# Kernel tuning notes

Measured on AMD Instinct MI355X. Metric: run time of the kernel, lower is better.

Reference implementation:

```python
import jax, jax.numpy as jnp
import numpy as np

TAU = 2.0      # LIF time constant
EPS = 1e-5     # BatchNorm eps
ALPHA = 4.0    # sigmoid surrogate-gradient sharpness (spikingjelly default)

@jax.custom_vjp
def _spike(x):
    return (x >= 0.0).astype(x.dtype)

def _spike_fwd(x):
    return _spike(x), x

def _spike_bwd(x, g):
    s = jax.nn.sigmoid(ALPHA * x)
    return (g * ALPHA * s * (1.0 - s),)

_spike.defvjp(_spike_fwd, _spike_bwd)

def lif(x_seq, v_th=1.0):
    # Multi-step LIF with hard reset to 0, detach_reset=True, v[0]=0.
    # x_seq: (T, ...) ; scan over T.
    def step(v, x):
        v = v + (x - v) / TAU
        s = _spike(v - v_th)
        v = v * (1.0 - jax.lax.stop_gradient(s))  # detach_reset
        return v, s
    _, s_seq = jax.lax.scan(step, jnp.zeros_like(x_seq[0]), x_seq)
    return s_seq

def bn(x, gamma, beta, mean, var):
    # inference-mode BatchNorm2d on (T,B,C,H,W), params (C,)
    sh = (1, 1, -1, 1, 1)
    scale = gamma.reshape(sh) * jax.lax.rsqrt(var.reshape(sh) + EPS)
    return (x - mean.reshape(sh)) * scale + beta.reshape(sh)

def conv1x1(x, w):
    # 1x1 conv == channel matmul; x: (T,B,C,H,W), w: (Cout,Cin)
    return jnp.einsum('tbchw,dc->tbdhw', x, w)

def setup_inputs() -> dict:
    key = jax.random.key(0)
    ks = jax.random.split(key, 24)
    T, B, C, H, W = 4, 32, 384, 16, 16
    d = {}
    d['x'] = jax.random.normal(ks[0], (T, B, C, H, W), jnp.float32)
    for i, p in enumerate(['q', 'k', 'v']):
        base = 1 + 5 * i
        d[p + '_w'] = jax.random.normal(ks[base], (C, C), jnp.float32) * 0.05
        d[p + '_gamma'] = jax.random.uniform(ks[base + 1], (C,), jnp.float32) + 0.5
        d[p + '_beta'] = jax.random.normal(ks[base + 2], (C,), jnp.float32) * 0.1
        d[p + '_mean'] = jax.random.normal(ks[base + 3], (C,), jnp.float32) * 0.1
        d[p + '_var'] = jax.random.uniform(ks[base + 4], (C,), jnp.float32) + 0.5
    d['proj_w'] = jax.random.normal(ks[16], (C, C), jnp.float32) * 0.05
    d['proj_b'] = jax.random.normal(ks[17], (C,), jnp.float32) * 0.1
    d['proj_gamma'] = jax.random.uniform(ks[18], (C,), jnp.float32) + 0.5
    d['proj_beta'] = jax.random.normal(ks[19], (C,), jnp.float32) * 0.1
    d['proj_mean'] = jax.random.normal(ks[20], (C,), jnp.float32) * 0.1
    d['proj_var'] = jax.random.uniform(ks[21], (C,), jnp.float32) + 0.5
    d['num_heads'] = 8
    return d

def reference(x, q_w, q_gamma, q_beta, q_mean, q_var,
              k_w, k_gamma, k_beta, k_mean, k_var,
              v_w, v_gamma, v_beta, v_mean, v_var,
              proj_w, proj_b, proj_gamma, proj_beta, proj_mean, proj_var,
              num_heads):
    T, B, C, H, W = x.shape
    N = H * W
    Ch = C // num_heads
    identity = x
    xs = lif(x)  # shortcut_lif

    def branch(w, g, b, m, var_):
        o = lif(bn(conv1x1(xs, w), g, b, m, var_))  # (T,B,C,H,W), binary spikes
        # flatten(3).transpose(-1,-2).reshape(T,B,N,h,Ch).permute -> (T,B,h,N,Ch)
        return o.reshape(T, B, num_heads, Ch, N).transpose(0, 1, 2, 4, 3)

    q = branch(q_w, q_gamma, q_beta, q_mean, q_var)
    k = branch(k_w, k_gamma, k_beta, k_mean, k_var)
    v = branch(v_w, v_gamma, v_beta, v_mean, v_var)

    kv = (k * v).sum(axis=3, keepdims=True)      # (T,B,h,1,Ch) linear-attn reduce over N
    kv = lif(kv, v_th=0.5)                       # talking_heads_lif
    y = q * kv                                   # (T,B,h,N,Ch)
    y = y.transpose(0, 1, 2, 4, 3).reshape(T, B, C, H, W)
    y = conv1x1(y, proj_w) + proj_b.reshape(1, 1, -1, 1, 1)
    y = bn(y, proj_gamma, proj_beta, proj_mean, proj_var)
    return (y + identity, v)
```

## Files before the change

### kernel.cpp

```cpp
#include <hip/hip_runtime.h>

typedef unsigned short u16;
typedef unsigned char u8;
typedef signed char i8;
typedef int i32x4 __attribute__((ext_vector_type(4)));
typedef int i32x16 __attribute__((ext_vector_type(16)));
typedef float f32x4 __attribute__((ext_vector_type(4)));
typedef unsigned u32x4 __attribute__((ext_vector_type(4)));
typedef u8 u8x16 __attribute__((ext_vector_type(16)));

#define CHS 2097152L

__device__ __forceinline__ void gload16(const void* g, void* l) {
    __builtin_amdgcn_global_load_lds(
        (const __attribute__((address_space(1))) void*)g,
        (__attribute__((address_space(3))) void*)l, 16, 0, 0);
}

__global__ __launch_bounds__(256) void prep(const float* __restrict__ X, u8* __restrict__ Xt,
    const float* __restrict__ qw, const float* __restrict__ kw,
    const float* __restrict__ vw, const float* __restrict__ pw,
    i8* __restrict__ Wq, float* __restrict__ Sc, float* __restrict__ KVraw) {
    const int bid = blockIdx.x;
    if (bid < 768) {
        __shared__ __attribute__((aligned(16))) u8 s2[4][32][136];
        const int c0 = (bid % 3) * 128;
        const int n0 = ((bid / 3) & 7) * 32;
        const int b = bid / 24;
        const int n4 = (threadIdx.x & 7) << 2;
        const int cl0 = threadIdx.x >> 3;
        #pragma unroll
        for (int pass = 0; pass < 4; pass++) {
            const int c_l = cl0 + (pass << 5);
            f32x4 vm = {0.f, 0.f, 0.f, 0.f};
            #pragma unroll
            for (int t = 0; t < 4; t++) {
                f32x4 xv = __builtin_nontemporal_load(
                    (const f32x4*)&X[(((long)t * 32 + b) * 384 + c0 + c_l) * 256 + n0 + n4]);
                #pragma unroll
                for (int e = 0; e < 4; e++) {
                    vm[e] += (xv[e] - vm[e]) * 0.5f;
                    u8 sp = 0;
                    if (vm[e] >= 1.0f) { sp = 1; vm[e] = 0.f; }
                    s2[t][n4 + e][c_l] = sp;
                }
            }
        }
        __syncthreads();
        const int c16 = (threadIdx.x & 7) << 4;
        const int n = (threadIdx.x >> 3) & 31;
        const int cglob = c0 + c16;
        const int ch = cglob >> 6, off = cglob & 63;
        #pragma unroll
        for (int t = 0; t < 4; t++) {
            u8x16 v = *(const u8x16*)&s2[t][n][c16];
            *(u8x16*)&Xt[(long)ch * CHS + ((long)(b * 256 + n0 + n) * 4 + t) * 64 + off] = v;
        }
    } else {
        const int wv = bid - 768;
        const int w = threadIdx.x >> 6, lane = threadIdx.x & 63;
        const int r = wv * 4 + w;
        const int m = r / 384, d = r - m * 384;
        const float* srcs[4] = {qw, kw, vw, pw};
        const float* row = srcs[m] + (long)d * 384;
        float a[6]; float mx = 0.f;
        #pragma unroll
        for (int jj = 0; jj < 6; jj++) { a[jj] = row[lane + (jj << 6)]; mx = fmaxf(mx, fabsf(a[jj])); }
        #pragma unroll
        for (int off = 1; off < 64; off <<= 1) mx = fmaxf(mx, __shfl_xor(mx, off));
        float scale = mx * (1.f / 127.f);
        float sinv = mx > 0.f ? 127.f / mx : 0.f;
        if (lane == 0) Sc[r] = scale;
        i8* dstb = Wq + (long)(m == 3 ? 9 : m * 3) * 147456 + (long)d * 64;
        #pragma unroll
        for (int jj = 0; jj < 6; jj++) {
            float x = a[jj] * sinv;
            float q1 = rintf(x);         float r1 = x - q1;
            float q2 = rintf(r1 * 128.f); float r2 = r1 * 128.f - q2;
            float q3 = rintf(r2 * 128.f);
            int co = jj * 24576 + lane;
            dstb[co] = (i8)(int)q1;
            dstb[147456 + co] = (i8)(int)q2;
            if (m != 3) dstb[2 * 147456 + co] = (i8)(int)q3;
        }
        const int idx = wv * 256 + threadIdx.x;
        if (idx < 49152) KVraw[idx] = 0.f;
    }
}

template<int NL>
__device__ __forceinline__ void gemm_i8(const u8* __restrict__ A, const i8* __restrict__ B,
                                        char* lds8, int m0, int n0, i32x16 (&acc)[NL][2]) {
    const int tid = threadIdx.x, l = tid & 63, w = tid >> 6;
    const int wm = (w & 1) << 6, wn = (w >> 1) << 5;
    const int col = l & 31, kg = l >> 5;
    const int rA = tid >> 2, sl = tid & 3;
    const int cs = (sl ^ ((rA >> 1) & 3)) << 4;
    const u8* Ap = A + (long)(m0 + rA) * 64 + cs;
    const i8* Bp = B + (long)(n0 + rA) * 64 + cs;
    const int BUFSZ = (2 + NL) * 4096;
    char* dst = lds8 + tid * 16;

    gload16(Ap, dst);
    gload16(Ap + 4096, dst + 4096);
    #pragma unroll
    for (int p = 0; p < NL; p++)
        gload16(Bp + p * 147456, dst + 8192 + p * 4096);

    for (int ck = 0; ck < 6; ck++) {
        const int cur = ck & 1;
        if (ck < 5) {
            char* d = dst + (cur ^ 1) * BUFSZ;
            gload16(Ap + (ck + 1) * CHS, d);
            gload16(Ap + (ck + 1) * CHS + 4096, d + 4096);
            #pragma unroll
            for (int p = 0; p < NL; p++)
                gload16(Bp + p * 147456 + (ck + 1) * 24576, d + 8192 + p * 4096);
            if (NL == 3) asm volatile("s_waitcnt vmcnt(5)" ::: "memory");
            else         asm volatile("s_waitcnt vmcnt(4)" ::: "memory");
        } else {
            asm volatile("s_waitcnt vmcnt(0)" ::: "memory");
        }
        __builtin_amdgcn_s_barrier();
        __builtin_amdgcn_sched_barrier(0);
        char* base = lds8 + cur * BUFSZ;
        #pragma unroll
        for (int c = 0; c < 2; c++) {
            i32x4 af[2];
            #pragma unroll
            for (int i = 0; i < 2; i++) {
                int ra = wm + (i << 5) + col;
                int sa = ((2 * c + kg) ^ ((ra >> 1) & 3)) << 4;
                af[i] = *(const i32x4*)(base + ra * 64 + sa);
            }
            int rb = wn + col;
            int sb = ((2 * c + kg) ^ ((rb >> 1) & 3)) << 4;
            #pragma unroll
            for (int p = 0; p < NL; p++) {
                i32x4 bf = *(const i32x4*)(base + 8192 + p * 4096 + rb * 64 + sb);
                #pragma unroll
                for (int i = 0; i < 2; i++)
                    acc[p][i] = __builtin_amdgcn_mfma_i32_32x32x32_i8(af[i], bf, acc[p][i], 0, 0, 0);
            }
        }
        __builtin_amdgcn_sched_barrier(0);
        __builtin_amdgcn_s_barrier();
    }
}

__global__ __launch_bounds__(256, 4) void k2(
    const u8* __restrict__ Xt, const i8* __restrict__ Wq, const float* __restrict__ Sc,
    const float* __restrict__ g0, const float* __restrict__ b0, const float* __restrict__ m0_, const float* __restrict__ v0_,
    const float* __restrict__ g1, const float* __restrict__ b1, const float* __restrict__ m1_, const float* __restrict__ v1_,
    const float* __restrict__ g2, const float* __restrict__ b2, const float* __restrict__ m2_, const float* __restrict__ v2_,
    u8* __restrict__ oq, u8* __restrict__ ok, u8* __restrict__ ov, float* __restrict__ out1)
{
    __shared__ __attribute__((aligned(16))) char lds8[40960];
    const int bid = blockIdx.x;
    const int xcd = bid & 7, bi = bid >> 3;
    const int mt = (bi / 18) * 8 + xcd;
    const int sub = bi % 18;
    const int m0 = mt * 128, d0 = (sub % 6) * 64, br = sub / 6;
    const float* G  = br == 0 ? g0  : (br == 1 ? g1  : g2);
    const float* Be = br == 0 ? b0  : (br == 1 ? b1  : b2);
    const float* Mu = br == 0 ? m0_ : (br == 1 ? m1_ : m2_);
    const float* Va = br == 0 ? v0_ : (br == 1 ? v1_ : v2_);

    i32x16 acc[3][2];
    #pragma unroll
    for (int p = 0; p < 3; p++)
        #pragma unroll
        for (int i = 0; i < 2; i++)
            #pragma unroll
            for (int r = 0; r < 16; r++) acc[p][i][r] = 0;
    gemm_i8<3>(Xt, Wq + (long)br * 3 * 147456, lds8, m0, d0, acc);

    const int tid = threadIdx.x, l = tid & 63, w = tid >> 6;
    const int wm = (w & 1) << 6, wn = (w >> 1) << 5;
    const int col = l & 31;
    const int d = d0 + wn + col;
    const float scb = G[d] / sqrtf(Va[d] + 1e-5f);
    const float mu = Mu[d], be = Be[d];
    const float wsc = Sc[br * 384 + d];
    u8* tile8 = (u8*)lds8;
    const float c1 = 0.0078125f, c2 = 6.103515625e-05f;
    #pragma unroll
    for (int i = 0; i < 2; i++)
        #pragma unroll
        for (int q = 0; q < 4; q++) {
            float vm = 0.f;
            int mb = wm + (i << 5) + (q << 3) + ((l >> 5) << 2);
            #pragma unroll
            for (int t = 0; t < 4; t++) {
                int reg = q * 4 + t;
                float f = (float)acc[0][i][reg] + (float)acc[1][i][reg] * c1
                        + (float)acc[2][i][reg] * c2;
                float bn = (f * wsc - mu) * scb + be;
                vm += (bn - vm) * 0.5f;
                u8 s = 0;
                if (vm >= 1.0f) { s = 1; vm = 0.f; }
                tile8[(mb + t) * 80 + wn + col] = s;
            }
        }
    __syncthreads();
    u8* Out8 = br == 0 ? oq : (br == 1 ? ok : ov);
    const long rbase = (long)(d0 >> 6) * CHS + (long)m0 * 64;
    u32x4 w0 = *(const u32x4*)&tile8[(tid >> 2) * 80 + ((tid & 3) << 4)];
    u32x4 w1 = *(const u32x4*)&tile8[(64 + (tid >> 2)) * 80 + ((tid & 3) << 4)];
    *(u32x4*)(Out8 + rbase + tid * 16) = w0;
    *(u32x4*)(Out8 + rbase + 4096 + tid * 16) = w1;
    if (br == 2) {
        const int b = m0 >> 10, n_base = (m0 >> 2) & 255;
        const int dl4 = (tid & 15) << 2;
        const int d2 = d0 + dl4;
        const int h = d2 / 48, chn = d2 - h * 48;
        #pragma unroll
        for (int q = 0; q < 8; q++) {
            int mlq = (tid >> 4) + (q << 4);
            int t = mlq & 3, n = n_base + (mlq >> 2);
            f32x4 v;
            #pragma unroll
            for (int r = 0; r < 4; r++) v[r] = tile8[mlq * 80 + dl4 + r] ? 1.0f : 0.f;
            long gi = ((((long)t * 32 + b) * 8 + h) * 256 + n) * 48 + chn;
            __builtin_nontemporal_store(v, (f32x4*)&out1[gi]);
        }
    }
}

__global__ __launch_bounds__(384) void k3a(const u8* __restrict__ Ks, const u8* __restrict__ Vs,
                                           float* __restrict__ kv_raw) {
    const int b = blockIdx.y, nc = blockIdx.x;
    const int d4 = threadIdx.x * 4, t = threadIdx.y;
    const long cbase = (long)(d4 >> 6) * CHS + (d4 & 63);
    int cnt0 = 0, cnt1 = 0, cnt2 = 0, cnt3 = 0;
    for (int nl = 0; nl < 32; nl++) {
        const long row = ((long)b * 256 + nc * 32 + nl) * 4 + t;
        uchar4 kk = *(const uchar4*)&Ks[cbase + row * 64];
        uchar4 vv = *(const uchar4*)&Vs[cbase + row * 64];
        cnt0 += (kk.x & vv.x); cnt1 += (kk.y & vv.y);
        cnt2 += (kk.z & vv.z); cnt3 += (kk.w & vv.w);
    }
    float* dst = &kv_raw[((long)t * 32 + b) * 384 + d4];
    atomicAdd(dst + 0, (float)cnt0);
    atomicAdd(dst + 1, (float)cnt1);
    atomicAdd(dst + 2, (float)cnt2);
    atomicAdd(dst + 3, (float)cnt3);
}

__global__ __launch_bounds__(256, 4) void k4(
    const u8* __restrict__ Qs, const float* __restrict__ kv_raw,
    const i8* __restrict__ Pq, const float* __restrict__ Scp,
    const float* __restrict__ PB, const float* __restrict__ PG, const float* __restrict__ PBe,
    const float* __restrict__ PM, const float* __restrict__ PV,
    const float* __restrict__ X, float* __restrict__ O)
{
    __shared__ __attribute__((aligned(16))) char lds8[35328];
    u8* kvs_s = (u8*)(lds8 + 33792);
    const int bid = blockIdx.x;
    const int xcd = bid & 7, bi = bid >> 3;
    const int mt = (bi / 6) * 8 + xcd;
    const int m0 = mt * 128, e0 = (bi % 6) * 64;
    const int tid = threadIdx.x;
    const int b = m0 >> 10;

    for (int dd = tid; dd < 384; dd += 256) {
        float vm = 0.f;
        #pragma unroll
        for (int t = 0; t < 4; t++) {
            vm += (kv_raw[((long)t * 32 + b) * 384 + dd] - vm) * 0.5f;
            u8 sp = 0;
            if (vm >= 0.5f) { sp = 1; vm = 0.f; }
            kvs_s[t * 384 + dd] = sp;
        }
    }
    __syncthreads();

    i32x16 acc[2][2];
    #pragma unroll
    for (int p = 0; p < 2; p++)
        #pragma unroll
        for (int i = 0; i < 2; i++)
            #pragma unroll
            for (int r = 0; r < 16; r++) acc[p][i][r] = 0;
    const int l = tid & 63, w = tid >> 6;
    const int wm = (w & 1) << 6, wn = (w >> 1) << 5;
    const int col = l & 31, kg = l >> 5;
    const int rA = tid >> 2, sl = tid & 3;
    const int cs = (sl ^ ((rA >> 1) & 3)) << 4;
    const int tA = rA & 3;
    const u8* Ap = Qs + (long)(m0 + rA) * 64 + cs;
    const i8* Bp = Pq + (long)(e0 + rA) * 64 + cs;
    const int BUFSZ = 16384;
    char* dst = lds8 + tid * 16;
    {
        u32x4 mk = *(const u32x4*)&kvs_s[tA * 384 + cs];
        u32x4 q0 = *(const u32x4*)(Ap);
        u32x4 q1 = *(const u32x4*)(Ap + 4096);
        gload16(Bp, dst + 8192);
        gload16(Bp + 147456, dst + 12288);
        *(u32x4*)dst = q0 & mk;
        *(u32x4*)(dst + 4096) = q1 & mk;
    }
    __syncthreads();
    for (int ck = 0; ck < 6; ck++) {
        const int cur = ck & 1;
        u32x4 qn0, qn1, mk;
        char* dn = dst + (cur ^ 1) * BUFSZ;
        if (ck < 5) {
            mk = *(const u32x4*)&kvs_s[tA * 384 + (ck + 1) * 64 + cs];
            qn0 = *(const u32x4*)(Ap + (ck + 1) * CHS);
            qn1 = *(const u32x4*)(Ap + (ck + 1) * CHS + 4096);
            gload16(Bp + (ck + 1) * 24576, dn + 8192);
            gload16(Bp + 147456 + (ck + 1) * 24576, dn + 12288);
        }
        char* base = lds8 + cur * BUFSZ;
        #pragma unroll
        for (int c = 0; c < 2; c++) {
            i32x4 af[2];
            #pragma unroll
            for (int i = 0; i < 2; i++) {
                int ra = wm + (i << 5) + col;
                int sa = ((2 * c + kg) ^ ((ra >> 1) & 3)) << 4;
                af[i] = *(const i32x4*)(base + ra * 64 + sa);
            }
            int rb = wn + col;
            int sb = ((2 * c + kg) ^ ((rb >> 1) & 3)) << 4;
            #pragma unroll
            for (int p = 0; p < 2; p++) {
                i32x4 bf = *(const i32x4*)(base + 8192 + p * 4096 + rb * 64 + sb);
                #pragma unroll
                for (int i = 0; i < 2; i++)
                    acc[p][i] = __builtin_amdgcn_mfma_i32_32x32x32_i8(af[i], bf, acc[p][i], 0, 0, 0);
            }
        }
        if (ck < 5) {
            *(u32x4*)dn = qn0 & mk;
            *(u32x4*)(dn + 4096) = qn1 & mk;
        }
        __syncthreads();
    }

    const int e = e0 + wn + col;
    const float scb = PG[e] / sqrtf(PV[e] + 1e-5f);
    const float mu = PM[e], be = PBe[e], pbb = PB[e];
    const float wsc = Scp[e];
    float* smemf = (float*)lds8;
    const float c1 = 0.0078125f;
    #pragma unroll
    for (int i = 0; i < 2; i++)
        #pragma unroll
        for (int q = 0; q < 4; q++)
            #pragma unroll
            for (int t = 0; t < 4; t++) {
                int reg = q * 4 + t;
                float f = (float)acc[0][i][reg] + (float)acc[1][i][reg] * c1;
                float z = (f * wsc + pbb - mu) * scb + be;
                int m = wm + (i << 5) + (q << 3) + ((l >> 5) << 2) + t;
                smemf[(wn + col) * 132 + m] = z;
            }
    __syncthreads();
    const int n_base = (m0 >> 2) & 255;
    const int n_l = tid & 31;
    #pragma unroll
    for (int ei = 0; ei < 8; ei++) {
        int e_l = (tid >> 5) + (ei << 3);
        f32x4 v = *(const f32x4*)&smemf[e_l * 132 + (n_l << 2)];
        #pragma unroll
        for (int t = 0; t < 4; t++) {
            long gi = (((long)t * 32 + b) * 384 + e0 + e_l) * 256 + n_base + n_l;
            float xv = __builtin_nontemporal_load(&X[gi]);
            __builtin_nontemporal_store(v[t] + xv, &O[gi]);
        }
    }
}

extern "C" void kernel_launch(void* const* d_in, const int* in_sizes, int n_in,
                              void* d_out, int out_size, void* d_ws, size_t ws_size,
                              hipStream_t stream) {
    (void)in_sizes; (void)n_in; (void)out_size; (void)ws_size;
    const float* x   = (const float*)d_in[0];
    const float* qw  = (const float*)d_in[1];
    const float* qg  = (const float*)d_in[2];
    const float* qb  = (const float*)d_in[3];
    const float* qm  = (const float*)d_in[4];
    const float* qv  = (const float*)d_in[5];
    const float* kw  = (const float*)d_in[6];
    const float* kg  = (const float*)d_in[7];
    const float* kb  = (const float*)d_in[8];
    const float* km  = (const float*)d_in[9];
    const float* kv  = (const float*)d_in[10];
    const float* vw  = (const float*)d_in[11];
    const float* vg  = (const float*)d_in[12];
    const float* vb  = (const float*)d_in[13];
    const float* vm  = (const float*)d_in[14];
    const float* vv  = (const float*)d_in[15];
    const float* pw  = (const float*)d_in[16];
    const float* pb  = (const float*)d_in[17];
    const float* pg  = (const float*)d_in[18];
    const float* pbe = (const float*)d_in[19];
    const float* pm  = (const float*)d_in[20];
    const float* pv  = (const float*)d_in[21];

    float* out0 = (float*)d_out;
    float* out1 = out0 + 12582912;
    char*  ob   = (char*)d_out;
    u8*    Qs8  = (u8*)ob;
    u8*    Xt8  = (u8*)(ob + 12582912);
    char*  ws   = (char*)d_ws;
    u8*    Ks8  = (u8*)ws;
    u8*    Vs8  = (u8*)ws + 12582912;
    float* KVraw = (float*)(ws + 25165824);
    i8*    Wq    = (i8*)(ws + 25411584);
    float* Sc    = (float*)(ws + 27033600);

    hipLaunchKernelGGL(prep, dim3(1152), dim3(256), 0, stream, x, Xt8, qw, kw, vw, pw, Wq, Sc, KVraw);
    hipLaunchKernelGGL(k2, dim3(4608), dim3(256), 0, stream,
                       Xt8, Wq, Sc,
                       qg, qb, qm, qv,
                       kg, kb, km, kv,
                       vg, vb, vm, vv,
                       Qs8, Ks8, Vs8, out1);
    hipLaunchKernelGGL(k3a, dim3(8, 32), dim3(96, 4), 0, stream, Ks8, Vs8, KVraw);
    hipLaunchKernelGGL(k4, dim3(1536), dim3(256), 0, stream,
                       Qs8, KVraw, Wq + 9 * 147456L, Sc + 3 * 384, pb, pg, pbe, pm, pv, x, out0);
}
```

Baseline: 262.0 us.

## Fuse K·V spike-count reduction into the K/V GEMM blocks and drop k3a

The k2 kernel now uses 3072 blocks. Q blocks run the Q GEMM alone, and combined blocks run the K GEMM then the V GEMM back to back. The K and V spikes are kept in per-lane bitmasks, ANDed, popcounted per timestep into shared counters, and atomically added to kv_raw. This removes the K/V spike write-back to workspace and the separate k3a reduction launch. The cost is that K/V blocks now do two GEMMs serially, which makes the load uneven between Q and K/V blocks.

```diff
diff --git a/kernel.cpp b/kernel.cpp
--- a/kernel.cpp
+++ b/kernel.cpp
@@ -3,6 +3,7 @@
 typedef unsigned short u16;
 typedef unsigned char u8;
 typedef signed char i8;
+typedef unsigned u32;
 typedef int i32x4 __attribute__((ext_vector_type(4)));
 typedef int i32x16 __attribute__((ext_vector_type(16)));
 typedef float f32x4 __attribute__((ext_vector_type(4)));
@@ -153,98 +154,146 @@
     const float* __restrict__ g0, const float* __restrict__ b0, const float* __restrict__ m0_, const float* __restrict__ v0_,
     const float* __restrict__ g1, const float* __restrict__ b1, const float* __restrict__ m1_, const float* __restrict__ v1_,
     const float* __restrict__ g2, const float* __restrict__ b2, const float* __restrict__ m2_, const float* __restrict__ v2_,
-    u8* __restrict__ oq, u8* __restrict__ ok, u8* __restrict__ ov, float* __restrict__ out1)
+    u8* __restrict__ oq, float* __restrict__ kv_raw, float* __restrict__ out1)
 {
     __shared__ __attribute__((aligned(16))) char lds8[40960];
+    __shared__ int cnt_s[4][64];
     const int bid = blockIdx.x;
     const int xcd = bid & 7, bi = bid >> 3;
-    const int mt = (bi / 18) * 8 + xcd;
-    const int sub = bi % 18;
-    const int m0 = mt * 128, d0 = (sub % 6) * 64, br = sub / 6;
-    const float* G  = br == 0 ? g0  : (br == 1 ? g1  : g2);
-    const float* Be = br == 0 ? b0  : (br == 1 ? b1  : b2);
-    const float* Mu = br == 0 ? m0_ : (br == 1 ? m1_ : m2_);
-    const float* Va = br == 0 ? v0_ : (br == 1 ? v1_ : v2_);
-
-    i32x16 acc[3][2];
-    #pragma unroll
-    for (int p = 0; p < 3; p++)
-        #pragma unroll
-        for (int i = 0; i < 2; i++)
-            #pragma unroll
-            for (int r = 0; r < 16; r++) acc[p][i][r] = 0;
-    gemm_i8<3>(Xt, Wq + (long)br * 3 * 147456, lds8, m0, d0, acc);
-
+    const int mt = (bi / 12) * 8 + xcd;
+    const int sub = bi % 12;
+    const int m0 = mt * 128, d0 = (sub % 6) * 64;
+    const int role = sub / 6;
     const int tid = threadIdx.x, l = tid & 63, w = tid >> 6;
     const int wm = (w & 1) << 6, wn = (w >> 1) << 5;
     const int col = l & 31;
     const int d = d0 + wn + col;
-    const float scb = G[d] / sqrtf(Va[d] + 1e-5f);
-    const float mu = Mu[d], be = Be[d];
-    const float wsc = Sc[br * 384 + d];
+    const int b = m0 >> 10;
     u8* tile8 = (u8*)lds8;
     const float c1 = 0.0078125f, c2 = 6.103515625e-05f;
-    #pragma unroll
-    for (int i = 0; i < 2; i++)
-        #pragma unroll
-        for (int q = 0; q < 4; q++) {
-            float vm = 0.f;
-            int mb = wm + (i << 5) + (q << 3) + ((l >> 5) << 2);
-            #pragma unroll
-            for (int t = 0; t < 4; t++) {
-                int reg = q * 4 + t;
-                float f = (float)acc[0][i][reg] + (float)acc[1][i][reg] * c1
-                        + (float)acc[2][i][reg] * c2;
-                float bn = (f * wsc - mu) * scb + be;
-                vm += (bn - vm) * 0.5f;
-                u8 s = 0;
-                if (vm >= 1.0f) { s = 1; vm = 0.f; }
-                tile8[(mb + t) * 80 + wn + col] = s;
-            }
-        }
-    __syncthreads();
-    u8* Out8 = br == 0 ? oq : (br == 1 ? ok : ov);
-    const long rbase = (long)(d0 >> 6) * CHS + (long)m0 * 64;
-    u32x4 w0 = *(const u32x4*)&tile8[(tid >> 2) * 80 + ((tid & 3) << 4)];
-    u32x4 w1 = *(const u32x4*)&tile8[(64 + (tid >> 2)) * 80 + ((tid & 3) << 4)];
-    *(u32x4*)(Out8 + rbase + tid * 16) = w0;
-    *(u32x4*)(Out8 + rbase + 4096 + tid * 16) = w1;
-    if (br == 2) {
-        const int b = m0 >> 10, n_base = (m0 >> 2) & 255;
-        const int dl4 = (tid & 15) << 2;
-        const int d2 = d0 + dl4;
-        const int h = d2 / 48, chn = d2 - h * 48;
-        #pragma unroll
-        for (int q = 0; q < 8; q++) {
-            int mlq = (tid >> 4) + (q << 4);
-            int t = mlq & 3, n = n_base + (mlq >> 2);
-            f32x4 v;
-            #pragma unroll
-            for (int r = 0; r < 4; r++) v[r] = tile8[mlq * 80 + dl4 + r] ? 1.0f : 0.f;
-            long gi = ((((long)t * 32 + b) * 8 + h) * 256 + n) * 48 + chn;
-            __builtin_nontemporal_store(v, (f32x4*)&out1[gi]);
-        }
-    }
-}
-
-__global__ __launch_bounds__(384) void k3a(const u8* __restrict__ Ks, const u8* __restrict__ Vs,
-                                           float* __restrict__ kv_raw) {
-    const int b = blockIdx.y, nc = blockIdx.x;
-    const int d4 = threadIdx.x * 4, t = threadIdx.y;
-    const long cbase = (long)(d4 >> 6) * CHS + (d4 & 63);
-    int cnt0 = 0, cnt1 = 0, cnt2 = 0, cnt3 = 0;
-    for (int nl = 0; nl < 32; nl++) {
-        const long row = ((long)b * 256 + nc * 32 + nl) * 4 + t;
-        uchar4 kk = *(const uchar4*)&Ks[cbase + row * 64];
-        uchar4 vv = *(const uchar4*)&Vs[cbase + row * 64];
-        cnt0 += (kk.x & vv.x); cnt1 += (kk.y & vv.y);
-        cnt2 += (kk.z & vv.z); cnt3 += (kk.w & vv.w);
-    }
-    float* dst = &kv_raw[((long)t * 32 + b) * 384 + d4];
-    atomicAdd(dst + 0, (float)cnt0);
-    atomicAdd(dst + 1, (float)cnt1);
-    atomicAdd(dst + 2, (float)cnt2);
-    atomicAdd(dst + 3, (float)cnt3);
+
+    i32x16 acc[3][2];
+    if (role == 0) {
+        #pragma unroll
+        for (int p = 0; p < 3; p++)
+            #pragma unroll
+            for (int i = 0; i < 2; i++)
+                #pragma unroll
+                for (int r = 0; r < 16; r++) acc[p][i][r] = 0;
+        gemm_i8<3>(Xt, Wq, lds8, m0, d0, acc);
+        const float scb = g0[d] / sqrtf(v0_[d] + 1e-5f);
+        const float mu = m0_[d], be = b0[d];
+        const float wsc = Sc[d];
+        #pragma unroll
+        for (int i = 0; i < 2; i++)
+            #pragma unroll
+            for (int q = 0; q < 4; q++) {
+                float vm = 0.f;
+                int mb = wm + (i << 5) + (q << 3) + ((l >> 5) << 2);
+                #pragma unroll
+                for (int t = 0; t < 4; t++) {
+                    int reg = q * 4 + t;
+                    float f = (float)acc[0][i][reg] + (float)acc[1][i][reg] * c1
+                            + (float)acc[2][i][reg] * c2;
+                    float bn = (f * wsc - mu) * scb + be;
+                    vm += (bn - vm) * 0.5f;
+                    u8 s = 0;
+                    if (vm >= 1.0f) { s = 1; vm = 0.f; }
+                    tile8[(mb + t) * 80 + wn + col] = s;
+                }
+            }
+        __syncthreads();
+        const long rbase = (long)(d0 >> 6) * CHS + (long)m0 * 64;
+        u32x4 w0 = *(const u32x4*)&tile8[(tid >> 2) * 80 + ((tid & 3) << 4)];
+        u32x4 w1 = *(const u32x4*)&tile8[(64 + (tid >> 2)) * 80 + ((tid & 3) << 4)];
+        *(u32x4*)(oq + rbase + tid * 16) = w0;
+        *(u32x4*)(oq + rbase + 4096 + tid * 16) = w1;
+    } else {
+        #pragma unroll
+        for (int p = 0; p < 3; p++)
+            #pragma unroll
+            for (int i = 0; i < 2; i++)
+                #pragma unroll
+                for (int r = 0; r < 16; r++) acc[p][i][r] = 0;
+        gemm_i8<3>(Xt, Wq + 3 * 147456, lds8, m0, d0, acc);
+        u32 kb = 0;
+        {
+            const float scb = g1[d] / sqrtf(v1_[d] + 1e-5f);
+            const float mu = m1_[d], be = b1[d];
+            const float wsc = Sc[384 + d];
+            #pragma unroll
+            for (int i = 0; i < 2; i++)
+                #pragma unroll
+                for (int q = 0; q < 4; q++) {
+                    float vm = 0.f;
+                    #pragma unroll
+                    for (int t = 0; t < 4; t++) {
+                        int reg = q * 4 + t;
+                        float f = (float)acc[0][i][reg] + (float)acc[1][i][reg] * c1
+                                + (float)acc[2][i][reg] * c2;
+                        float bn = (f * wsc - mu) * scb + be;
+                        vm += (bn - vm) * 0.5f;
+                        if (vm >= 1.0f) { kb |= 1u << ((i << 4) | (q << 2) | t); vm = 0.f; }
+                    }
+                }
+        }
+        #pragma unroll
+        for (int p = 0; p < 3; p++)
+            #pragma unroll
+            for (int i = 0; i < 2; i++)
+                #pragma unroll
+                for (int r = 0; r < 16; r++) acc[p][i][r] = 0;
+        gemm_i8<3>(Xt, Wq + 6 * 147456, lds8, m0, d0, acc);
+        u32 vb = 0;
+        {
+            const float scb = g2[d] / sqrtf(v2_[d] + 1e-5f);
+            const float mu = m2_[d], be = b2[d];
+            const float wsc = Sc[768 + d];
+            #pragma unroll
+            for (int i = 0; i < 2; i++)
+                #pragma unroll
+                for (int q = 0; q < 4; q++) {
+                    float vm = 0.f;
+                    int mb = wm + (i << 5) + (q << 3) + ((l >> 5) << 2);
+                    #pragma unroll
+                    for (int t = 0; t < 4; t++) {
+                        int reg = q * 4 + t;
+                        float f = (float)acc[0][i][reg] + (float)acc[1][i][reg] * c1
+                                + (float)acc[2][i][reg] * c2;
+                        float bn = (f * wsc - mu) * scb + be;
+                        vm += (bn - vm) * 0.5f;
+                        u8 s = 0;
+                        if (vm >= 1.0f) { s = 1; vb |= 1u << ((i << 4) | (q << 2) | t); vm = 0.f; }
+                        tile8[(mb + t) * 80 + wn + col] = s;
+                    }
+                }
+        }
+        cnt_s[tid >> 6][tid & 63] = 0;
+        __syncthreads();
+        const u32 both = kb & vb;
+        #pragma unroll
+        for (int t = 0; t < 4; t++)
+            atomicAdd(&cnt_s[t][wn + col], __builtin_popcount(both & (0x11111111u << t)));
+        {
+            const int n_base = (m0 >> 2) & 255;
+            const int dl4 = (tid & 15) << 2;
+            const int d2 = d0 + dl4;
+            const int h = d2 / 48, chn = d2 - h * 48;
+            #pragma unroll
+            for (int q = 0; q < 8; q++) {
+                int mlq = (tid >> 4) + (q << 4);
+                int t = mlq & 3, n = n_base + (mlq >> 2);
+                f32x4 v;
+                #pragma unroll
+                for (int r = 0; r < 4; r++) v[r] = tile8[mlq * 80 + dl4 + r] ? 1.0f : 0.f;
+                long gi = ((((long)t * 32 + b) * 8 + h) * 256 + n) * 48 + chn;
+                __builtin_nontemporal_store(v, (f32x4*)&out1[gi]);
+            }
+        }
+        __syncthreads();
+        atomicAdd(&kv_raw[((long)(tid >> 6) * 32 + b) * 384 + d0 + (tid & 63)],
+                  (float)cnt_s[tid >> 6][tid & 63]);
+    }
 }
 
 __global__ __launch_bounds__(256, 4) void k4(
@@ -407,20 +456,17 @@
     u8*    Qs8  = (u8*)ob;
     u8*    Xt8  = (u8*)(ob + 12582912);
     char*  ws   = (char*)d_ws;
-    u8*    Ks8  = (u8*)ws;
-    u8*    Vs8  = (u8*)ws + 12582912;
     float* KVraw = (float*)(ws + 25165824);
     i8*    Wq    = (i8*)(ws + 25411584);
     float* Sc    = (float*)(ws + 27033600);
 
     hipLaunchKernelGGL(prep, dim3(1152), dim3(256), 0, stream, x, Xt8, qw, kw, vw, pw, Wq, Sc, KVraw);
-    hipLaunchKernelGGL(k2, dim3(4608), dim3(256), 0, stream,
+    hipLaunchKernelGGL(k2, dim3(3072), dim3(256), 0, stream,
                        Xt8, Wq, Sc,
                        qg, qb, qm, qv,
                        kg, kb, km, kv,
                        vg, vb, vm, vv,
-                       Qs8, Ks8, Vs8, out1);
-    hipLaunchKernelGGL(k3a, dim3(8, 32), dim3(96, 4), 0, stream, Ks8, Vs8, KVraw);
+                       Qs8, KVraw, out1);
     hipLaunchKernelGGL(k4, dim3(1536), dim3(256), 0, stream,
                        Qs8, KVraw, Wq + 9 * 147456L, Sc + 3 * 384, pb, pg, pbe, pm, pv, x, out0);
 }
```

New measurement: 303.1 us. 1.16x slower.
